# Kernel optimization log

Measured on AMD Instinct MI355X. Metric: run time of the kernel, lower is better.

## Reference

```python
import jax, jax.numpy as jnp
from jax import lax
import numpy as np

B, T, D, U, C = 256, 512, 300, 64, 45


def setup_inputs() -> dict:
    key = jax.random.key(0)
    ks = jax.random.split(key, 6)
    x = jax.random.normal(ks[0], (B, T, D), dtype=jnp.float32)
    kernel = jax.random.normal(ks[1], (D, 3 * U), dtype=jnp.float32) * 0.05
    recurrent_kernel = jax.random.normal(ks[2], (U, 3 * U), dtype=jnp.float32) * 0.05
    bias = jax.random.normal(ks[3], (2, 3 * U), dtype=jnp.float32) * 0.05  # [input_bias, recurrent_bias]
    dense_w = jax.random.normal(ks[4], (U, C), dtype=jnp.float32) * 0.05
    dense_b = jnp.zeros((C,), dtype=jnp.float32)
    return {"x": x, "kernel": kernel, "recurrent_kernel": recurrent_kernel,
            "bias": bias, "dense_w": dense_w, "dense_b": dense_b}


def reference(x, kernel, recurrent_kernel, bias, dense_w, dense_b):
    # Keras GRU v2, reset_after=True, recurrent_activation=sigmoid, activation=relu
    b_sz, t_sz, _ = x.shape
    u = recurrent_kernel.shape[0]
    # Precompute all input projections once: [B,T,3U] -> scan over time [T,B,3U]
    mx = jnp.einsum('btd,dk->btk', x, kernel) + bias[0]
    mx = jnp.moveaxis(mx, 1, 0)
    rec_bias = bias[1]

    def step(h, mxt):
        mi = h @ recurrent_kernel + rec_bias          # [B,3U]
        xz, xr, xh = jnp.split(mxt, 3, axis=-1)
        rz, rr, rh = jnp.split(mi, 3, axis=-1)
        z = jax.nn.sigmoid(xz + rz)                   # update gate
        r = jax.nn.sigmoid(xr + rr)                   # reset gate
        hh = jax.nn.relu(xh + r * rh)                 # candidate (relu activation)
        h_new = z * h + (1.0 - z) * hh
        return h_new, h_new

    h0 = jnp.zeros((b_sz, u), dtype=x.dtype)
    _, hs = lax.scan(step, h0, mx)                    # [T,B,U]
    hs = jnp.moveaxis(hs, 0, 1)                       # [B,T,U]
    logits = hs @ dense_w + dense_b                   # [B,T,C]
    return jax.nn.softmax(logits, axis=-1)
```

## Files before the change

### kernel.cpp

```cpp
#include <hip/hip_runtime.h>
#include <math.h>

#define B_ 256
#define T_ 512
#define D_ 300
#define U_ 64
#define C_ 45

typedef _Float16 half_t;
typedef __attribute__((ext_vector_type(2))) _Float16 f16x2;
typedef __attribute__((ext_vector_type(8))) _Float16 f16x8;
typedef __attribute__((ext_vector_type(4))) float f32x4;

#define KSTEPS 10
#define NTILES 12

#if __has_builtin(__builtin_amdgcn_rcpf)
#define FRCP(x) __builtin_amdgcn_rcpf(x)
#else
#define FRCP(x) (1.0f / (x))
#endif

static __device__ inline float fdot2_(f16x2 a, f16x2 b, float c) {
#if __has_builtin(__builtin_amdgcn_fdot2)
    return __builtin_amdgcn_fdot2(a, b, c, false);
#else
    return fmaf((float)a.x, (float)b.x, fmaf((float)a.y, (float)b.y, c));
#endif
}

__global__ __launch_bounds__(256) void prep_kernel(
    const float* __restrict__ w,
    half_t* __restrict__ wt_hi,
    half_t* __restrict__ wt_lo)
{
    const int idx = blockIdx.x * 256 + threadIdx.x;
    if (idx >= KSTEPS * NTILES * 64) return;
    const int l  = idx & 63;
    const int nt = (idx >> 6) % NTILES;
    const int ks = idx / (64 * NTILES);
    const int col   = nt * 16 + (l & 15);
    const int kbase = ks * 32 + (l >> 4) * 8;

    half_t hi[8], lo[8];
#pragma unroll
    for (int e = 0; e < 8; ++e) {
        const int k = kbase + e;
        const float v = (k < D_) ? w[(size_t)k * 192 + col] : 0.f;
        const half_t h = (half_t)v;
        hi[e] = h;
        lo[e] = (half_t)(v - (float)h);
    }
    *(f16x8*)(wt_hi + (size_t)idx * 8) = *(const f16x8*)hi;
    *(f16x8*)(wt_lo + (size_t)idx * 8) = *(const f16x8*)lo;
}

__global__ __launch_bounds__(256, 4) void proj_kernel(
    const float*  __restrict__ x,
    const half_t* __restrict__ wt_hi,
    const half_t* __restrict__ wt_lo,
    const float*  __restrict__ bias,
    float* __restrict__ mx)
{
    const int tid  = threadIdx.x;
    const int l    = tid & 63;
    const int wv   = tid >> 6;
    const int lrow = l & 15;
    const int g    = l >> 4;
    const int m0   = blockIdx.x * 64;

    f32x4 acc[4][3];
#pragma unroll
    for (int ni = 0; ni < 3; ++ni) {
        const float b = bias[wv * 48 + ni * 16 + lrow];
        const f32x4 bv = {b, b, b, b};
#pragma unroll
        for (int mi = 0; mi < 4; ++mi) acc[mi][ni] = bv;
    }

    for (int ks = 0; ks < KSTEPS; ++ks) {
        f16x8 bhi[3], blo[3];
#pragma unroll
        for (int ni = 0; ni < 3; ++ni) {
            const size_t off = ((size_t)(ks * NTILES + wv * 3 + ni) * 64 + l) * 8;
            bhi[ni] = *(const f16x8*)(wt_hi + off);
            blo[ni] = *(const f16x8*)(wt_lo + off);
        }
#pragma unroll
        for (int mi = 0; mi < 4; ++mi) {
            const float* xr = x + (size_t)(m0 + mi * 16 + lrow) * D_ + ks * 32 + g * 8;
            float xv[8];
            if (ks < 9) {
                const float4 v0 = ((const float4*)xr)[0];
                const float4 v1 = ((const float4*)xr)[1];
                xv[0] = v0.x; xv[1] = v0.y; xv[2] = v0.z; xv[3] = v0.w;
                xv[4] = v1.x; xv[5] = v1.y; xv[6] = v1.z; xv[7] = v1.w;
            } else {
                const int kb = 288 + g * 8;
#pragma unroll
                for (int e = 0; e < 8; ++e) xv[e] = (kb + e < D_) ? xr[e] : 0.f;
            }
            f16x8 ahi, alo;
#pragma unroll
            for (int e = 0; e < 8; ++e) {
                const half_t h = (half_t)xv[e];
                ahi[e] = h;
                alo[e] = (half_t)(xv[e] - (float)h);
            }
#pragma unroll
            for (int ni = 0; ni < 3; ++ni) {
                acc[mi][ni] = __builtin_amdgcn_mfma_f32_16x16x32_f16(ahi, bhi[ni], acc[mi][ni], 0, 0, 0);
                acc[mi][ni] = __builtin_amdgcn_mfma_f32_16x16x32_f16(alo, bhi[ni], acc[mi][ni], 0, 0, 0);
                acc[mi][ni] = __builtin_amdgcn_mfma_f32_16x16x32_f16(ahi, blo[ni], acc[mi][ni], 0, 0, 0);
            }
        }
    }

#pragma unroll
    for (int mi = 0; mi < 4; ++mi) {
        const int rbase = m0 + mi * 16 + g * 4;
#pragma unroll
        for (int ni = 0; ni < 3; ++ni) {
            const int col = wv * 48 + ni * 16 + lrow;
#pragma unroll
            for (int r = 0; r < 4; ++r)
                mx[(size_t)(rbase + r) * 192 + col] = acc[mi][ni][r];
        }
    }
}

__global__ __launch_bounds__(64) void scan_kernel(
    const float* __restrict__ mx,
    const float* __restrict__ rk,
    const float* __restrict__ bias,
    float* __restrict__ hs)
{
    __shared__ _Float16 hbuf[64];
    const int j = threadIdx.x;
    const int b = blockIdx.x;

    f16x2 Rz[32], Rr[32], Rh[32];
#pragma unroll
    for (int p = 0; p < 32; ++p) {
        Rz[p] = f16x2{(_Float16)rk[(size_t)(2 * p) * 192 + j],
                      (_Float16)rk[(size_t)(2 * p + 1) * 192 + j]};
        Rr[p] = f16x2{(_Float16)rk[(size_t)(2 * p) * 192 + 64 + j],
                      (_Float16)rk[(size_t)(2 * p + 1) * 192 + 64 + j]};
        Rh[p] = f16x2{(_Float16)rk[(size_t)(2 * p) * 192 + 128 + j],
                      (_Float16)rk[(size_t)(2 * p + 1) * 192 + 128 + j]};
    }
    const float rbz = bias[192 + j];
    const float rbr = bias[192 + 64 + j];
    const float rbh = bias[192 + 128 + j];

    hbuf[j] = (_Float16)0.f;
    float hj = 0.f;

    const float* mxb = mx + (size_t)b * T_ * 192 + j;
    float* hsb = hs + (size_t)b * T_ * 64 + j;

    float zb[4], rbv[4], qb[4];
#pragma unroll
    for (int i = 0; i < 4; ++i) {
        const float* p = mxb + (size_t)i * 192;
        zb[i] = p[0]; rbv[i] = p[64]; qb[i] = p[128];
    }

    union H8 { f16x8 v; f16x2 p[4]; };

    for (int t0 = 0; t0 < T_; t0 += 4) {
#pragma unroll
        for (int i = 0; i < 4; ++i) {
            const int t = t0 + i;
            const float xz = zb[i], xr = rbv[i], xh = qb[i];
            {
                const int tp = (t + 4 < T_) ? (t + 4) : (T_ - 1);
                const float* pf = mxb + (size_t)tp * 192;
                zb[i] = pf[0]; rbv[i] = pf[64]; qb[i] = pf[128];
            }
            H8 hv[8];
            const f16x8* h8 = (const f16x8*)hbuf;
#pragma unroll
            for (int q = 0; q < 8; ++q) hv[q].v = h8[q];

            float az[4] = {rbz, 0.f, 0.f, 0.f};
            float ar[4] = {rbr, 0.f, 0.f, 0.f};
            float ah[4] = {rbh, 0.f, 0.f, 0.f};
#pragma unroll
            for (int p = 0; p < 32; ++p) {
                const f16x2 hp = hv[p >> 2].p[p & 3];
                az[p & 3] = fdot2_(hp, Rz[p], az[p & 3]);
                ar[p & 3] = fdot2_(hp, Rr[p], ar[p & 3]);
                ah[p & 3] = fdot2_(hp, Rh[p], ah[p & 3]);
            }
            const float miz = (az[0] + az[1]) + (az[2] + az[3]);
            const float mir = (ar[0] + ar[1]) + (ar[2] + ar[3]);
            const float mih = (ah[0] + ah[1]) + (ah[2] + ah[3]);

            const float zg = FRCP(1.f + __expf(-(xz + miz)));
            const float rg = FRCP(1.f + __expf(-(xr + mir)));
            const float hh = fmaxf(fmaf(rg, mih, xh), 0.f);
            const float hn = fmaf(zg, hj - hh, hh);

            hbuf[j] = (_Float16)hn;
            hj = hn;
            hsb[(size_t)t * 64] = hn;
        }
    }
}

__global__ __launch_bounds__(256) void head_kernel(
    const float* __restrict__ hs,
    const half_t* __restrict__ dwt,
    const float* __restrict__ db,
    float* __restrict__ out)
{
    const int l    = threadIdx.x & 63;
    const int wv   = threadIdx.x >> 6;
    const int lrow = l & 15;
    const int g    = l >> 4;

    f16x8 bf[2][3];
#pragma unroll
    for (int ks2 = 0; ks2 < 2; ++ks2)
#pragma unroll
        for (int nt = 0; nt < 3; ++nt)
            bf[ks2][nt] = *(const f16x8*)(dwt + (size_t)((ks2 * 3 + nt) * 64 + l) * 8);
    float dbl[3];
#pragma unroll
    for (int nt = 0; nt < 3; ++nt) {
        const int col = nt * 16 + lrow;
        dbl[nt] = (col < C_) ? db[col] : 0.f;
    }

    const int gw = blockIdx.x * 4 + wv;
    const int nw = gridDim.x * 4;
    const int NTILE_M = (B_ * T_) / 16;
    for (int tile = gw; tile < NTILE_M; tile += nw) {
        const int m0 = tile * 16;
        const float* ar = hs + (size_t)(m0 + lrow) * 64 + g * 8;
        const float4 v0 = ((const float4*)ar)[0];
        const float4 v1 = ((const float4*)ar)[1];
        const float4 v2 = ((const float4*)(ar + 32))[0];
        const float4 v3 = ((const float4*)(ar + 32))[1];
        f16x8 a0, a1;
        a0[0] = (_Float16)v0.x; a0[1] = (_Float16)v0.y; a0[2] = (_Float16)v0.z; a0[3] = (_Float16)v0.w;
        a0[4] = (_Float16)v1.x; a0[5] = (_Float16)v1.y; a0[6] = (_Float16)v1.z; a0[7] = (_Float16)v1.w;
        a1[0] = (_Float16)v2.x; a1[1] = (_Float16)v2.y; a1[2] = (_Float16)v2.z; a1[3] = (_Float16)v2.w;
        a1[4] = (_Float16)v3.x; a1[5] = (_Float16)v3.y; a1[6] = (_Float16)v3.z; a1[7] = (_Float16)v3.w;

        f32x4 acc[3];
#pragma unroll
        for (int nt = 0; nt < 3; ++nt) {
            acc[nt] = f32x4{dbl[nt], dbl[nt], dbl[nt], dbl[nt]};
            acc[nt] = __builtin_amdgcn_mfma_f32_16x16x32_f16(a0, bf[0][nt], acc[nt], 0, 0, 0);
            acc[nt] = __builtin_amdgcn_mfma_f32_16x16x32_f16(a1, bf[1][nt], acc[nt], 0, 0, 0);
        }

#pragma unroll
        for (int r = 0; r < 4; ++r) {
            const float v0r = acc[0][r];
            const float v1r = acc[1][r];
            const float v2r = (lrow < 13) ? acc[2][r] : -INFINITY;
            float mxv = fmaxf(fmaxf(v0r, v1r), v2r);
#pragma unroll
            for (int s = 1; s < 16; s <<= 1) mxv = fmaxf(mxv, __shfl_xor(mxv, s, 64));
            const float e0 = __expf(v0r - mxv);
            const float e1 = __expf(v1r - mxv);
            const float e2 = (lrow < 13) ? __expf(acc[2][r] - mxv) : 0.f;
            float ssum = e0 + e1 + e2;
#pragma unroll
            for (int s = 1; s < 16; s <<= 1) ssum += __shfl_xor(ssum, s, 64);
            const float inv = 1.f / ssum;

            float* o = out + (size_t)(m0 + 4 * g + r) * C_;
            o[lrow]      = e0 * inv;
            o[16 + lrow] = e1 * inv;
            if (lrow < 13) o[32 + lrow] = e2 * inv;
        }
    }
}

__global__ __launch_bounds__(256) void prep2_kernel(
    const float* __restrict__ dw,
    half_t* __restrict__ dwt)
{
    const int idx = blockIdx.x * 256 + threadIdx.x;
    if (idx >= 2 * 3 * 64) return;
    const int l   = idx & 63;
    const int nt  = (idx >> 6) % 3;
    const int ks2 = idx / (64 * 3);
    const int col = nt * 16 + (l & 15);
    const int kb  = ks2 * 32 + (l >> 4) * 8;

    half_t v[8];
#pragma unroll
    for (int e = 0; e < 8; ++e) {
        const float f = (col < C_) ? dw[(size_t)(kb + e) * C_ + col] : 0.f;
        v[e] = (half_t)f;
    }
    *(f16x8*)(dwt + (size_t)idx * 8) = *(const f16x8*)v;
}

__global__ __launch_bounds__(256) void fused_kernel(
    const float*  __restrict__ x,
    const half_t* __restrict__ wt_hi,
    const half_t* __restrict__ wt_lo,
    const float*  __restrict__ bias,
    const float*  __restrict__ rk,
    float* __restrict__ hs)
{
    __shared__ float mxbuf[2][64][192];
    __shared__ _Float16 hbuf[64];
    const int tid = threadIdx.x;
    const int wv  = tid >> 6;
    const int l   = tid & 63;
    const int b   = blockIdx.x;

    if (wv == 0) {
        const int j = l;
        f16x2 Rz[32], Rr[32], Rh[32];
#pragma unroll
        for (int p = 0; p < 32; ++p) {
            Rz[p] = f16x2{(_Float16)rk[(size_t)(2 * p) * 192 + j],
                          (_Float16)rk[(size_t)(2 * p + 1) * 192 + j]};
            Rr[p] = f16x2{(_Float16)rk[(size_t)(2 * p) * 192 + 64 + j],
                          (_Float16)rk[(size_t)(2 * p + 1) * 192 + 64 + j]};
            Rh[p] = f16x2{(_Float16)rk[(size_t)(2 * p) * 192 + 128 + j],
                          (_Float16)rk[(size_t)(2 * p + 1) * 192 + 128 + j]};
        }
        const float rbz = bias[192 + j];
        const float rbr = bias[192 + 64 + j];
        const float rbh = bias[192 + 128 + j];

        hbuf[j] = (_Float16)0.f;
        float hj = 0.f;
        float* hsb = hs + (size_t)b * T_ * 64 + j;

        union H8 { f16x8 v; f16x2 p[4]; };
        __syncthreads();

        for (int c = 0; c < 8; ++c) {
            const float (*mb)[192] = mxbuf[c & 1];
            float z0 = mb[0][j], r0 = mb[0][64 + j], q0 = mb[0][128 + j];
            float z1 = mb[1][j], r1 = mb[1][64 + j], q1 = mb[1][128 + j];

            for (int tt = 0; tt < 64; tt += 2) {
#pragma unroll
                for (int i = 0; i < 2; ++i) {
                    const float xz = (i == 0) ? z0 : z1;
                    const float xr = (i == 0) ? r0 : r1;
                    const float xh = (i == 0) ? q0 : q1;
                    const int tp = (tt + 2 + i < 64) ? (tt + 2 + i) : 63;
                    const float zn = mb[tp][j];
                    const float rn = mb[tp][64 + j];
                    const float qn = mb[tp][128 + j];

                    H8 hv[8];
                    const f16x8* h8 = (const f16x8*)hbuf;
#pragma unroll
                    for (int q = 0; q < 8; ++q) hv[q].v = h8[q];

                    float az[4] = {rbz, 0.f, 0.f, 0.f};
                    float ar[4] = {rbr, 0.f, 0.f, 0.f};
                    float ah[4] = {rbh, 0.f, 0.f, 0.f};
#pragma unroll
                    for (int p = 0; p < 32; ++p) {
                        const f16x2 hp = hv[p >> 2].p[p & 3];
                        az[p & 3] = fdot2_(hp, Rz[p], az[p & 3]);
                        ar[p & 3] = fdot2_(hp, Rr[p], ar[p & 3]);
                        ah[p & 3] = fdot2_(hp, Rh[p], ah[p & 3]);
                    }
                    const float miz = (az[0] + az[1]) + (az[2] + az[3]);
                    const float mir = (ar[0] + ar[1]) + (ar[2] + ar[3]);
                    const float mih = (ah[0] + ah[1]) + (ah[2] + ah[3]);

                    const float zg = FRCP(1.f + __expf(-(xz + miz)));
                    const float rg = FRCP(1.f + __expf(-(xr + mir)));
                    const float hh = fmaxf(fmaf(rg, mih, xh), 0.f);
                    const float hn = fmaf(zg, hj - hh, hh);

                    hbuf[j] = (_Float16)hn;
                    hj = hn;
                    hsb[(size_t)(c * 64 + tt + i) * 64] = hn;

                    if (i == 0) { z0 = zn; r0 = rn; q0 = qn; }
                    else        { z1 = zn; r1 = rn; q1 = qn; }
                }
            }
            __syncthreads();
        }
    } else {
        const int pw   = wv - 1;
        const int lrow = l & 15;
        const int g    = l >> 4;
        float b0[4];
#pragma unroll
        for (int q = 0; q < 4; ++q) b0[q] = bias[(pw * 4 + q) * 16 + lrow];

        auto produce = [&](int c) {
            const int t0 = c * 64;
            f32x4 acc[4][4];
#pragma unroll
            for (int mi = 0; mi < 4; ++mi)
#pragma unroll
                for (int q = 0; q < 4; ++q)
                    acc[mi][q] = f32x4{b0[q], b0[q], b0[q], b0[q]};

            for (int ks = 0; ks < KSTEPS; ++ks) {
                f16x8 bh[4], bl[4];
#pragma unroll
                for (int q = 0; q < 4; ++q) {
                    const size_t off = ((size_t)(ks * NTILES + pw * 4 + q) * 64 + l) * 8;
                    bh[q] = *(const f16x8*)(wt_hi + off);
                    bl[q] = *(const f16x8*)(wt_lo + off);
                }
#pragma unroll
                for (int mi = 0; mi < 4; ++mi) {
                    const float* xr = x + (size_t)(b * 512 + t0 + mi * 16 + lrow) * D_ + ks * 32 + g * 8;
                    float xv[8];
                    if (ks < 9) {
                        const float4 v0 = ((const float4*)xr)[0];
                        const float4 v1 = ((const float4*)xr)[1];
                        xv[0] = v0.x; xv[1] = v0.y; xv[2] = v0.z; xv[3] = v0.w;
                        xv[4] = v1.x; xv[5] = v1.y; xv[6] = v1.z; xv[7] = v1.w;
                    } else {
                        const int kb = 288 + g * 8;
#pragma unroll
                        for (int e = 0; e < 8; ++e) xv[e] = (kb + e < D_) ? xr[e] : 0.f;
                    }
                    f16x8 ahi, alo;
#pragma unroll
                    for (int e = 0; e < 8; ++e) {
                        const half_t h = (half_t)xv[e];
                        ahi[e] = h;
                        alo[e] = (half_t)(xv[e] - (float)h);
                    }
#pragma unroll
                    for (int q = 0; q < 4; ++q) {
                        acc[mi][q] = __builtin_amdgcn_mfma_f32_16x16x32_f16(ahi, bh[q], acc[mi][q], 0, 0, 0);
                        acc[mi][q] = __builtin_amdgcn_mfma_f32_16x16x32_f16(alo, bh[q], acc[mi][q], 0, 0, 0);
                        acc[mi][q] = __builtin_amdgcn_mfma_f32_16x16x32_f16(ahi, bl[q], acc[mi][q], 0, 0, 0);
                    }
                }
            }
            const int cb = c & 1;
#pragma unroll
            for (int mi = 0; mi < 4; ++mi)
#pragma unroll
                for (int q = 0; q < 4; ++q) {
                    const int col = (pw * 4 + q) * 16 + lrow;
#pragma unroll
                    for (int r = 0; r < 4; ++r)
                        mxbuf[cb][mi * 16 + 4 * g + r][col] = acc[mi][q][r];
                }
        };

        produce(0);
        __syncthreads();
        for (int c = 0; c < 8; ++c) {
            if (c < 7) produce(c + 1);
            __syncthreads();
        }
    }
}

extern "C" void kernel_launch(void* const* d_in, const int* in_sizes, int n_in,
                              void* d_out, int out_size, void* d_ws, size_t ws_size,
                              hipStream_t stream) {
    const float* x  = (const float*)d_in[0];
    const float* w  = (const float*)d_in[1];
    const float* rk = (const float*)d_in[2];
    const float* bs = (const float*)d_in[3];
    const float* dw = (const float*)d_in[4];
    const float* db = (const float*)d_in[5];
    float* out = (float*)d_out;

    char* ws = (char*)d_ws;
    float*  hs    = (float*)(ws + (size_t)131072 * 192 * 4);
    half_t* wt_hi = (half_t*)(ws + (size_t)131072 * 256 * 4);
    half_t* wt_lo = wt_hi + (size_t)KSTEPS * NTILES * 64 * 8;
    half_t* dwt   = wt_lo + (size_t)KSTEPS * NTILES * 64 * 8;

    prep_kernel <<<30,   256, 0, stream>>>(w, wt_hi, wt_lo);
    prep2_kernel<<<2,    256, 0, stream>>>(dw, dwt);
    fused_kernel<<<256,  256, 0, stream>>>(x, wt_hi, wt_lo, bs, rk, hs);
    head_kernel <<<1024, 256, 0, stream>>>(hs, dwt, db, out);
}
```

Measured before the change: 196.4 us.

## Compute GRU recurrent matvec with MFMA instead of per-lane fdot2

The serial recurrence wave now computes h @ recurrent_kernel with 16x16x32 f16 MFMA instructions over 12 column tiles, holding the recurrent weights as MFMA B-fragments in registers. Only the first row of each output tile is meaningful (h is broadcast as a single row), and only lanes 0-15 write the new hidden state. This replaces 96 dependent fdot2 ops per lane per step with 24 MFMAs, aiming to shorten the latency-bound serial critical path. In exchange most of each MFMA's work is wasted, MFMA latency sits on the dependency chain, and the per-step gate loads now cover 12 columns per lane.

```diff
diff --git a/kernel.cpp b/kernel.cpp
--- a/kernel.cpp
+++ b/kernel.cpp
@@ -311,81 +311,74 @@
     float* __restrict__ hs)
 {
     __shared__ float mxbuf[2][64][192];
-    __shared__ _Float16 hbuf[64];
+    __shared__ __align__(16) _Float16 hb16[64];
     const int tid = threadIdx.x;
     const int wv  = tid >> 6;
     const int l   = tid & 63;
     const int b   = blockIdx.x;
 
     if (wv == 0) {
-        const int j = l;
-        f16x2 Rz[32], Rr[32], Rh[32];
-#pragma unroll
-        for (int p = 0; p < 32; ++p) {
-            Rz[p] = f16x2{(_Float16)rk[(size_t)(2 * p) * 192 + j],
-                          (_Float16)rk[(size_t)(2 * p + 1) * 192 + j]};
-            Rr[p] = f16x2{(_Float16)rk[(size_t)(2 * p) * 192 + 64 + j],
-                          (_Float16)rk[(size_t)(2 * p + 1) * 192 + 64 + j]};
-            Rh[p] = f16x2{(_Float16)rk[(size_t)(2 * p) * 192 + 128 + j],
-                          (_Float16)rk[(size_t)(2 * p + 1) * 192 + 128 + j]};
-        }
-        const float rbz = bias[192 + j];
-        const float rbr = bias[192 + 64 + j];
-        const float rbh = bias[192 + 128 + j];
-
-        hbuf[j] = (_Float16)0.f;
-        float hj = 0.f;
-        float* hsb = hs + (size_t)b * T_ * 64 + j;
-
-        union H8 { f16x8 v; f16x2 p[4]; };
+        const int ll = l & 15;
+        const int g  = l >> 4;
+
+        f16x8 Rf[NTILES][2];
+#pragma unroll
+        for (int nt = 0; nt < NTILES; ++nt)
+#pragma unroll
+            for (int kf = 0; kf < 2; ++kf) {
+                f16x8 v;
+#pragma unroll
+                for (int e = 0; e < 8; ++e)
+                    v[e] = (_Float16)rk[(size_t)(kf * 32 + g * 8 + e) * 192 + nt * 16 + ll];
+                Rf[nt][kf] = v;
+            }
+        float rb[NTILES];
+#pragma unroll
+        for (int nt = 0; nt < NTILES; ++nt) rb[nt] = bias[192 + nt * 16 + ll];
+
+        hb16[l] = (_Float16)0.f;
+        float hj[4] = {0.f, 0.f, 0.f, 0.f};
+        float* hsb = hs + (size_t)b * T_ * 64 + ll;
+
         __syncthreads();
 
         for (int c = 0; c < 8; ++c) {
             const float (*mb)[192] = mxbuf[c & 1];
-            float z0 = mb[0][j], r0 = mb[0][64 + j], q0 = mb[0][128 + j];
-            float z1 = mb[1][j], r1 = mb[1][64 + j], q1 = mb[1][128 + j];
-
-            for (int tt = 0; tt < 64; tt += 2) {
-#pragma unroll
-                for (int i = 0; i < 2; ++i) {
-                    const float xz = (i == 0) ? z0 : z1;
-                    const float xr = (i == 0) ? r0 : r1;
-                    const float xh = (i == 0) ? q0 : q1;
-                    const int tp = (tt + 2 + i < 64) ? (tt + 2 + i) : 63;
-                    const float zn = mb[tp][j];
-                    const float rn = mb[tp][64 + j];
-                    const float qn = mb[tp][128 + j];
-
-                    H8 hv[8];
-                    const f16x8* h8 = (const f16x8*)hbuf;
-#pragma unroll
-                    for (int q = 0; q < 8; ++q) hv[q].v = h8[q];
-
-                    float az[4] = {rbz, 0.f, 0.f, 0.f};
-                    float ar[4] = {rbr, 0.f, 0.f, 0.f};
-                    float ah[4] = {rbh, 0.f, 0.f, 0.f};
-#pragma unroll
-                    for (int p = 0; p < 32; ++p) {
-                        const f16x2 hp = hv[p >> 2].p[p & 3];
-                        az[p & 3] = fdot2_(hp, Rz[p], az[p & 3]);
-                        ar[p & 3] = fdot2_(hp, Rr[p], ar[p & 3]);
-                        ah[p & 3] = fdot2_(hp, Rh[p], ah[p & 3]);
-                    }
-                    const float miz = (az[0] + az[1]) + (az[2] + az[3]);
-                    const float mir = (ar[0] + ar[1]) + (ar[2] + ar[3]);
-                    const float mih = (ah[0] + ah[1]) + (ah[2] + ah[3]);
-
-                    const float zg = FRCP(1.f + __expf(-(xz + miz)));
-                    const float rg = FRCP(1.f + __expf(-(xr + mir)));
-                    const float hh = fmaxf(fmaf(rg, mih, xh), 0.f);
-                    const float hn = fmaf(zg, hj - hh, hh);
-
-                    hbuf[j] = (_Float16)hn;
-                    hj = hn;
-                    hsb[(size_t)(c * 64 + tt + i) * 64] = hn;
-
-                    if (i == 0) { z0 = zn; r0 = rn; q0 = qn; }
-                    else        { z1 = zn; r1 = rn; q1 = qn; }
+            for (int tt = 0; tt < 64; ++tt) {
+                float mxv[NTILES];
+#pragma unroll
+                for (int nt = 0; nt < NTILES; ++nt) mxv[nt] = mb[tt][nt * 16 + ll];
+
+                const f16x8 a0 = *(const f16x8*)(hb16 + g * 8);
+                const f16x8 a1 = *(const f16x8*)(hb16 + 32 + g * 8);
+
+                f32x4 acc[NTILES];
+#pragma unroll
+                for (int nt = 0; nt < NTILES; ++nt)
+                    acc[nt] = __builtin_amdgcn_mfma_f32_16x16x32_f16(
+                        a0, Rf[nt][0], f32x4{0.f, 0.f, 0.f, 0.f}, 0, 0, 0);
+#pragma unroll
+                for (int nt = 0; nt < NTILES; ++nt)
+                    acc[nt] = __builtin_amdgcn_mfma_f32_16x16x32_f16(
+                        a1, Rf[nt][1], acc[nt], 0, 0, 0);
+
+#pragma unroll
+                for (int q = 0; q < 4; ++q) {
+                    const float sz = acc[q][0] + rb[q] + mxv[q];
+                    const float zg = FRCP(1.f + __expf(-sz));
+                    const float sr = acc[4 + q][0] + rb[4 + q] + mxv[4 + q];
+                    const float rg = FRCP(1.f + __expf(-sr));
+                    const float rh = acc[8 + q][0] + rb[8 + q];
+                    const float hh = fmaxf(fmaf(rg, rh, mxv[8 + q]), 0.f);
+                    hj[q] = fmaf(zg, hj[q] - hh, hh);
+                }
+
+                if (l < 16) {
+#pragma unroll
+                    for (int q = 0; q < 4; ++q) hb16[q * 16 + ll] = (_Float16)hj[q];
+                    float* hrow = hsb + (size_t)(c * 64 + tt) * 64;
+#pragma unroll
+                    for (int q = 0; q < 4; ++q) hrow[q * 16] = hj[q];
                 }
             }
             __syncthreads();
```

Result: slower. 245.3 us (+24.9%).
